# Performance work log

Hardware: AMD Instinct MI355X
Metric: run time of the kernel (lower is better)

## Reference

```python
import jax, jax.numpy as jnp
import numpy as np

# NAM: in_features independent 1->H->H->1 MLPs (FeatureNNs), batched over the
# feature dimension F instead of a Python loop of tiny kernels.
# inputs: (B, F); W1,b1: (F, H); W2: (F, H, H); b2: (F, H); W3: (F, H); b3: (F,)

def setup_inputs() -> dict:
    key = jax.random.key(0)
    ks = jax.random.split(key, 7)
    B, F, H = 8192, 128, 64
    s1 = 1.0  # fan_in = 1 for first layer
    s2 = 1.0 / np.sqrt(H)
    return {
        "inputs": jax.random.normal(ks[0], (B, F), dtype=jnp.float32),
        "W1": jax.random.normal(ks[1], (F, H), dtype=jnp.float32) * s1,
        "b1": jax.random.normal(ks[2], (F, H), dtype=jnp.float32) * 0.01,
        "W2": jax.random.normal(ks[3], (F, H, H), dtype=jnp.float32) * s2,
        "b2": jax.random.normal(ks[4], (F, H), dtype=jnp.float32) * 0.01,
        "W3": jax.random.normal(ks[5], (F, H), dtype=jnp.float32) * s2,
        "b3": jax.random.normal(ks[6], (F,), dtype=jnp.float32) * 0.01,
    }


def reference(inputs, W1, b1, W2, b2, W3, b3):
    # Layer 1: scalar input per feature -> hidden.  (B,F,1)*(F,H) -> (B,F,H)
    h1 = jax.nn.relu(inputs[:, :, None] * W1[None, :, :] + b1[None, :, :])
    # Layer 2: per-feature hidden->hidden batched matmul.
    h2 = jax.nn.relu(jnp.einsum("bfh,fhk->bfk", h1, W2) + b2[None, :, :])
    # Output layer: hidden -> scalar per feature.
    fnn = jnp.einsum("bfh,fh->bf", h2, W3) + b3[None, :]  # (B, F)
    out = fnn.sum(axis=-1)  # (B,)  additive model output
    return (out, fnn)
```

## Files before the change

### kernel.cpp

```cpp
#include <hip/hip_runtime.h>

#define B 8192
#define F 128
#define H 64

typedef __attribute__((ext_vector_type(8))) short bf16x8;
typedef __attribute__((ext_vector_type(4))) float f32x4;

static __device__ __forceinline__ unsigned short f32_to_bf16_rne(float v) {
    unsigned int u = __float_as_uint(v);
    unsigned int r = (u + 0x7FFFu + ((u >> 16) & 1u)) >> 16;
    return (unsigned short)r;
}
static __device__ __forceinline__ float bf16_to_f32(unsigned short h) {
    return __uint_as_float(((unsigned int)h) << 16);
}

#define GLOAD_LDS16(gp, lp)                                                  \
    __builtin_amdgcn_global_load_lds(                                        \
        (const __attribute__((address_space(1))) unsigned int*)(gp),         \
        (__attribute__((address_space(3))) unsigned int*)(lp), 16, 0, 0)


__global__ __launch_bounds__(256) void nam_prep(
    const float* __restrict__ inputs, const float* __restrict__ W2,
    short* __restrict__ bhi_g, short* __restrict__ blo_g,
    float* __restrict__ xT)
{
    const int tid = threadIdx.x;
    const int blk = blockIdx.x;
    __shared__ float tile[32][65];
    if (blk < 512) {
        const int r0 = (blk & 127) * 64;
        const int f0 = (blk >> 7) * 32;
#pragma unroll
        for (int j = 0; j < 8; ++j) {
            const int rl = j * 8 + (tid >> 5);
            const int fl = tid & 31;
            tile[fl][rl] = inputs[(size_t)(r0 + rl) * F + f0 + fl];
        }
        __syncthreads();
#pragma unroll
        for (int j = 0; j < 8; ++j) {
            const int fl = j * 4 + (tid >> 6);
            const int rl = tid & 63;
            xT[(size_t)(f0 + fl) * B + r0 + rl] = tile[fl][rl];
        }
    } else {
        const int f = blk - 512;
        const float* W2f = W2 + (size_t)f * H * H;
        short* bhi = bhi_g + (size_t)f * 4096;
        short* blo = blo_g + (size_t)f * 4096;
#pragma unroll
        for (int t = tid; t < 512; t += 256) {
            const int n = t & 63;
            const int g = t >> 6;
            const int nt = n >> 4, c = n & 15;
            const int ks = g >> 2, q = g & 3;
            const int slot = (nt * 2 + ks) * 64 + c + 16 * q;
            bf16x8 hv, lv;
#pragma unroll
            for (int jj = 0; jj < 8; ++jj) {
                const float wv = W2f[(g * 8 + jj) * H + n];
                const unsigned short hi = f32_to_bf16_rne(wv);
                const unsigned short lo = f32_to_bf16_rne(wv - bf16_to_f32(hi));
                hv[jj] = (short)hi;
                lv[jj] = (short)lo;
            }
            *(bf16x8*)&bhi[slot * 8] = hv;
            *(bf16x8*)&blo[slot * 8] = lv;
        }
    }
}

__global__ __launch_bounds__(256, 3) void nam_main(
    const float* __restrict__ xT, const float* __restrict__ W1,
    const float* __restrict__ b1, const short* __restrict__ bhi_g,
    const short* __restrict__ blo_g, const float* __restrict__ b2,
    const float* __restrict__ W3, const float* __restrict__ b3,
    float* __restrict__ fnn_ws)
{
    const int tid = threadIdx.x;
    const int f = blockIdx.y;
    const int b0 = blockIdx.x * 256;

    const int lane = tid & 63;
    const int w    = tid >> 6;
    const int q    = lane >> 4;
    const int col  = lane & 15;

    __shared__ __align__(16) short bhs[4096];
    __shared__ __align__(16) short bls[4096];
    {
        const short* bhi_f = bhi_g + (size_t)f * 4096;
        const short* blo_f = blo_g + (size_t)f * 4096;
#pragma unroll
        for (int c = w; c < 8; c += 4) {
            GLOAD_LDS16(bhi_f + c * 512 + lane * 8, &bhs[c * 512]);
            GLOAD_LDS16(blo_f + c * 512 + lane * 8, &bls[c * 512]);
        }
    }

    float x4[4];
#pragma unroll
    for (int mt = 0; mt < 4; ++mt)
        x4[mt] = xT[(size_t)f * B + b0 + w * 64 + mt * 16 + col];

    const float* W1f = W1 + f * H;
    const float* b1f = b1 + f * H;
    float w1v[16], b1v[16];
#pragma unroll
    for (int ks = 0; ks < 2; ++ks)
#pragma unroll
        for (int j = 0; j < 8; ++j) {
            w1v[ks * 8 + j] = W1f[ks * 32 + q * 8 + j];
            b1v[ks * 8 + j] = b1f[ks * 32 + q * 8 + j];
        }
    const float* b2f = b2 + f * H;
    const float* W3f = W3 + f * H;
    float b2v[4], w3v[4];
#pragma unroll
    for (int nt = 0; nt < 4; ++nt) {
        b2v[nt] = b2f[nt * 16 + col];
        w3v[nt] = W3f[nt * 16 + col];
    }
    const float b3f = b3[f];

    __syncthreads();

    bf16x8 bhi[4][2], blo[4][2];
#pragma unroll
    for (int nt = 0; nt < 4; ++nt)
#pragma unroll
        for (int ks = 0; ks < 2; ++ks) {
            const int slot = (nt * 2 + ks) * 64 + lane;
            bhi[nt][ks] = *(bf16x8*)&bhs[slot * 8];
            blo[nt][ks] = *(bf16x8*)&bls[slot * 8];
        }

#pragma unroll 1
    for (int mt = 0; mt < 4; ++mt) {
        const int rbase = b0 + w * 64 + mt * 16;
        const float x = x4[mt];

        f32x4 acc[4];
#pragma unroll
        for (int nt = 0; nt < 4; ++nt) {
            acc[nt][0] = b2v[nt]; acc[nt][1] = b2v[nt];
            acc[nt][2] = b2v[nt]; acc[nt][3] = b2v[nt];
        }

#pragma unroll
        for (int ks = 0; ks < 2; ++ks) {
            union { unsigned int u[4]; bf16x8 v; } Ah, Al;
#pragma unroll
            for (int t = 0; t < 4; ++t) {
                const float r0 = fmaxf(fmaf(x, w1v[ks * 8 + 2 * t],     b1v[ks * 8 + 2 * t]),     0.0f);
                const float r1 = fmaxf(fmaf(x, w1v[ks * 8 + 2 * t + 1], b1v[ks * 8 + 2 * t + 1]), 0.0f);
                const unsigned int u0 = __float_as_uint(r0);
                const unsigned int u1 = __float_as_uint(r1);
                const float l0 = r0 - __uint_as_float(u0 & 0xFFFF0000u);
                const float l1 = r1 - __uint_as_float(u1 & 0xFFFF0000u);
                Ah.u[t] = __builtin_amdgcn_perm(u1, u0, 0x07060302);
                Al.u[t] = __builtin_amdgcn_perm(__float_as_uint(l1),
                                                __float_as_uint(l0), 0x07060302);
            }
#pragma unroll
            for (int nt = 0; nt < 4; ++nt) {
                acc[nt] = __builtin_amdgcn_mfma_f32_16x16x32_bf16(Ah.v, bhi[nt][ks], acc[nt], 0, 0, 0);
                acc[nt] = __builtin_amdgcn_mfma_f32_16x16x32_bf16(Ah.v, blo[nt][ks], acc[nt], 0, 0, 0);
                acc[nt] = __builtin_amdgcn_mfma_f32_16x16x32_bf16(Al.v, bhi[nt][ks], acc[nt], 0, 0, 0);
            }
        }

        float s[4];
#pragma unroll
        for (int reg = 0; reg < 4; ++reg) {
            float t = 0.0f;
#pragma unroll
            for (int nt = 0; nt < 4; ++nt)
                t = fmaf(fmaxf(acc[nt][reg], 0.0f), w3v[nt], t);
            s[reg] = t;
        }
#pragma unroll
        for (int m_ = 1; m_ <= 8; m_ <<= 1)
#pragma unroll
            for (int reg = 0; reg < 4; ++reg)
                s[reg] += __shfl_xor(s[reg], m_, 64);
        if (col == 0) {
            f32x4 o;
            o[0] = s[0] + b3f; o[1] = s[1] + b3f;
            o[2] = s[2] + b3f; o[3] = s[3] + b3f;
            *(f32x4*)&fnn_ws[(size_t)f * B + rbase + 4 * q] = o;
        }
    }
}

__global__ __launch_bounds__(256) void nam_finish(
    const float* __restrict__ fnn_ws, float* __restrict__ fnn,
    float* __restrict__ out)
{
    const int tid = threadIdx.x;
    const int blk = blockIdx.x;
    const int r0 = (blk & 127) * 64;
    const int f0 = (blk >> 7) * 32;
    __shared__ float tile[32][65];
    __shared__ float psum[4][64];

    float rsum = 0.0f;
#pragma unroll
    for (int j = 0; j < 8; ++j) {
        const int fl = j * 4 + (tid >> 6);
        const int rl = tid & 63;
        const float v = fnn_ws[(size_t)(f0 + fl) * B + r0 + rl];
        tile[fl][rl] = v;
        rsum += v;
    }
    psum[tid >> 6][tid & 63] = rsum;
    __syncthreads();
    if (tid < 64) {
        const float s = psum[0][tid] + psum[1][tid] + psum[2][tid] + psum[3][tid];
        atomicAdd(&out[r0 + tid], s);
    }
#pragma unroll
    for (int j = 0; j < 8; ++j) {
        const int rl = j * 8 + (tid >> 5);
        const int fl = tid & 31;
        fnn[(size_t)(r0 + rl) * F + f0 + fl] = tile[fl][rl];
    }
}

__global__ __launch_bounds__(256, 3) void nam_mono(
    const float* __restrict__ inputs, const float* __restrict__ W1,
    const float* __restrict__ b1, const float* __restrict__ W2,
    const float* __restrict__ b2, const float* __restrict__ W3,
    const float* __restrict__ b3, float* __restrict__ out,
    float* __restrict__ fnn_out)
{
    const int tid = threadIdx.x;
    const int f = blockIdx.y;
    const int b0 = blockIdx.x * 256;

    const float* W1f = W1 + f * H;
    const float* b1f = b1 + f * H;
    const float* W2f = W2 + (size_t)f * H * H;
    const float* b2f = b2 + f * H;
    const float* W3f = W3 + f * H;

    __shared__ __align__(16) short bhi_s[512 * 8];
    __shared__ __align__(16) short blo_s[512 * 8];

#pragma unroll
    for (int t = tid; t < 512; t += 256) {
        const int n = t & 63;
        const int g = t >> 6;
        const int nt = n >> 4, c = n & 15;
        const int ks = g >> 2, q = g & 3;
        const int slot = (nt * 2 + ks) * 64 + c + 16 * q;
        bf16x8 hv, lv;
#pragma unroll
        for (int jj = 0; jj < 8; ++jj) {
            const float wv = W2f[(g * 8 + jj) * H + n];
            const unsigned short hi = f32_to_bf16_rne(wv);
            const unsigned short lo = f32_to_bf16_rne(wv - bf16_to_f32(hi));
            hv[jj] = (short)hi;
            lv[jj] = (short)lo;
        }
        *(bf16x8*)&bhi_s[slot * 8] = hv;
        *(bf16x8*)&blo_s[slot * 8] = lv;
    }

    const int lane = tid & 63;
    const int w    = tid >> 6;
    const int q    = lane >> 4;
    const int col  = lane & 15;

    float w1v[16], b1v[16];
#pragma unroll
    for (int ks = 0; ks < 2; ++ks)
#pragma unroll
        for (int j = 0; j < 8; ++j) {
            w1v[ks * 8 + j] = W1f[ks * 32 + q * 8 + j];
            b1v[ks * 8 + j] = b1f[ks * 32 + q * 8 + j];
        }
    float b2v[4], w3v[4];
#pragma unroll
    for (int nt = 0; nt < 4; ++nt) {
        b2v[nt] = b2f[nt * 16 + col];
        w3v[nt] = W3f[nt * 16 + col];
    }
    const float b3f = b3[f];

    float x4[4];
#pragma unroll
    for (int mt = 0; mt < 4; ++mt)
        x4[mt] = inputs[(size_t)(b0 + w * 64 + mt * 16 + col) * F + f];

    __syncthreads();

    bf16x8 bhi[4][2], blo[4][2];
#pragma unroll
    for (int nt = 0; nt < 4; ++nt)
#pragma unroll
        for (int ks = 0; ks < 2; ++ks) {
            const int slot = (nt * 2 + ks) * 64 + lane;
            bhi[nt][ks] = *(bf16x8*)&bhi_s[slot * 8];
            blo[nt][ks] = *(bf16x8*)&blo_s[slot * 8];
        }

#pragma unroll 1
    for (int mt = 0; mt < 4; ++mt) {
        const int rbase = b0 + w * 64 + mt * 16;
        const float x = x4[mt];

        f32x4 acc[4];
#pragma unroll
        for (int nt = 0; nt < 4; ++nt) {
            acc[nt][0] = b2v[nt]; acc[nt][1] = b2v[nt];
            acc[nt][2] = b2v[nt]; acc[nt][3] = b2v[nt];
        }

#pragma unroll
        for (int ks = 0; ks < 2; ++ks) {
            union { unsigned int u[4]; bf16x8 v; } Ah, Al;
#pragma unroll
            for (int t = 0; t < 4; ++t) {
                const float r0 = fmaxf(fmaf(x, w1v[ks * 8 + 2 * t],     b1v[ks * 8 + 2 * t]),     0.0f);
                const float r1 = fmaxf(fmaf(x, w1v[ks * 8 + 2 * t + 1], b1v[ks * 8 + 2 * t + 1]), 0.0f);
                const unsigned int u0 = __float_as_uint(r0);
                const unsigned int u1 = __float_as_uint(r1);
                const float l0 = r0 - __uint_as_float(u0 & 0xFFFF0000u);
                const float l1 = r1 - __uint_as_float(u1 & 0xFFFF0000u);
                Ah.u[t] = __builtin_amdgcn_perm(u1, u0, 0x07060302);
                Al.u[t] = __builtin_amdgcn_perm(__float_as_uint(l1),
                                                __float_as_uint(l0), 0x07060302);
            }
#pragma unroll
            for (int nt = 0; nt < 4; ++nt) {
                acc[nt] = __builtin_amdgcn_mfma_f32_16x16x32_bf16(Ah.v, bhi[nt][ks], acc[nt], 0, 0, 0);
                acc[nt] = __builtin_amdgcn_mfma_f32_16x16x32_bf16(Ah.v, blo[nt][ks], acc[nt], 0, 0, 0);
                acc[nt] = __builtin_amdgcn_mfma_f32_16x16x32_bf16(Al.v, bhi[nt][ks], acc[nt], 0, 0, 0);
            }
        }

        float s[4];
#pragma unroll
        for (int reg = 0; reg < 4; ++reg) {
            float t = 0.0f;
#pragma unroll
            for (int nt = 0; nt < 4; ++nt)
                t = fmaf(fmaxf(acc[nt][reg], 0.0f), w3v[nt], t);
            s[reg] = t;
        }
#pragma unroll
        for (int m_ = 1; m_ <= 8; m_ <<= 1)
#pragma unroll
            for (int reg = 0; reg < 4; ++reg)
                s[reg] += __shfl_xor(s[reg], m_, 64);
        if (col == 0) {
#pragma unroll
            for (int reg = 0; reg < 4; ++reg) {
                const int row = rbase + 4 * q + reg;
                const float val = s[reg] + b3f;
                fnn_out[(size_t)row * F + f] = val;
                atomicAdd(&out[row], val);
            }
        }
    }
}

extern "C" void kernel_launch(void* const* d_in, const int* in_sizes, int n_in,
                              void* d_out, int out_size, void* d_ws, size_t ws_size,
                              hipStream_t stream) {
    const float* inputs = (const float*)d_in[0];
    const float* W1     = (const float*)d_in[1];
    const float* b1     = (const float*)d_in[2];
    const float* W2     = (const float*)d_in[3];
    const float* b2     = (const float*)d_in[4];
    const float* W3     = (const float*)d_in[5];
    const float* b3     = (const float*)d_in[6];

    float* out = (float*)d_out;
    float* fnn = out + B;

    const size_t WS_NEEDED = (size_t)F * 4096 * 2 * sizeof(short)
                           + (size_t)F * B * 2 * sizeof(float);

    hipMemsetAsync(out, 0, B * sizeof(float), stream);

    if (ws_size >= WS_NEEDED) {
        short* bhi_g = (short*)d_ws;
        short* blo_g = bhi_g + (size_t)F * 4096;
        float* xT    = (float*)(blo_g + (size_t)F * 4096);
        float* fnw   = xT + (size_t)F * B;

        nam_prep<<<dim3(512 + F), 256, 0, stream>>>(inputs, W2, bhi_g, blo_g, xT);
        nam_main<<<dim3(B / 256, F), 256, 0, stream>>>(xT, W1, b1, bhi_g, blo_g,
                                                       b2, W3, b3, fnw);
        nam_finish<<<dim3(512), 256, 0, stream>>>(fnw, fnn, out);
    } else {
        nam_mono<<<dim3(B / 256, F), 256, 0, stream>>>(inputs, W1, b1, W2, b2,
                                                       W3, b3, out, fnn);
    }
}
```

Measured before the change: 107.5 us.

## Drop input transpose pass, read inputs strided in main kernel, raise occupancy

Removes the transpose of inputs into a feature-major workspace buffer from the prep kernel, so prep now only converts W2 into hi/lo bf16 fragments. The main kernel reads each x value straight from the row-major inputs with stride F, which saves a full read and write of the 4 MB input array but makes those loads uncoalesced. It also raises the launch-bounds occupancy hint from 3 to 4 blocks and unrolls the row-tile loop by 2, which adds register pressure. There is a harmless redundant self-assignment line in the lo conversion.

```diff
diff --git a/kernel.cpp b/kernel.cpp
--- a/kernel.cpp
+++ b/kernel.cpp
@@ -23,58 +23,38 @@
 
 
 __global__ __launch_bounds__(256) void nam_prep(
-    const float* __restrict__ inputs, const float* __restrict__ W2,
-    short* __restrict__ bhi_g, short* __restrict__ blo_g,
-    float* __restrict__ xT)
+    const float* __restrict__ W2, short* __restrict__ bhi_g,
+    short* __restrict__ blo_g)
 {
     const int tid = threadIdx.x;
-    const int blk = blockIdx.x;
-    __shared__ float tile[32][65];
-    if (blk < 512) {
-        const int r0 = (blk & 127) * 64;
-        const int f0 = (blk >> 7) * 32;
-#pragma unroll
-        for (int j = 0; j < 8; ++j) {
-            const int rl = j * 8 + (tid >> 5);
-            const int fl = tid & 31;
-            tile[fl][rl] = inputs[(size_t)(r0 + rl) * F + f0 + fl];
-        }
-        __syncthreads();
-#pragma unroll
-        for (int j = 0; j < 8; ++j) {
-            const int fl = j * 4 + (tid >> 6);
-            const int rl = tid & 63;
-            xT[(size_t)(f0 + fl) * B + r0 + rl] = tile[fl][rl];
-        }
-    } else {
-        const int f = blk - 512;
-        const float* W2f = W2 + (size_t)f * H * H;
-        short* bhi = bhi_g + (size_t)f * 4096;
-        short* blo = blo_g + (size_t)f * 4096;
-#pragma unroll
-        for (int t = tid; t < 512; t += 256) {
-            const int n = t & 63;
-            const int g = t >> 6;
-            const int nt = n >> 4, c = n & 15;
-            const int ks = g >> 2, q = g & 3;
-            const int slot = (nt * 2 + ks) * 64 + c + 16 * q;
-            bf16x8 hv, lv;
-#pragma unroll
-            for (int jj = 0; jj < 8; ++jj) {
-                const float wv = W2f[(g * 8 + jj) * H + n];
-                const unsigned short hi = f32_to_bf16_rne(wv);
-                const unsigned short lo = f32_to_bf16_rne(wv - bf16_to_f32(hi));
-                hv[jj] = (short)hi;
-                lv[jj] = (short)lo;
-            }
-            *(bf16x8*)&bhi[slot * 8] = hv;
-            *(bf16x8*)&blo[slot * 8] = lv;
-        }
-    }
-}
-
-__global__ __launch_bounds__(256, 3) void nam_main(
-    const float* __restrict__ xT, const float* __restrict__ W1,
+    const int f = blockIdx.x;
+    const float* W2f = W2 + (size_t)f * H * H;
+    short* bhi = bhi_g + (size_t)f * 4096;
+    short* blo = blo_g + (size_t)f * 4096;
+#pragma unroll
+    for (int t = tid; t < 512; t += 256) {
+        const int n = t & 63;
+        const int g = t >> 6;
+        const int nt = n >> 4, c = n & 15;
+        const int ks = g >> 2, q = g & 3;
+        const int slot = (nt * 2 + ks) * 64 + c + 16 * q;
+        bf16x8 hv, lv;
+#pragma unroll
+        for (int jj = 0; jj < 8; ++jj) {
+            const float wv = W2f[(g * 8 + jj) * H + n];
+            const unsigned short hi = f32_to_bf16_rne(wv);
+            const unsigned short lo = f32_to_bf16_rne(wv - bf16_to_f32(hi));
+            hv[jj] = (short)hi;
+            lv[jj] = (short)lv[jj];
+            lv[jj] = (short)lo;
+        }
+        *(bf16x8*)&bhi[slot * 8] = hv;
+        *(bf16x8*)&blo[slot * 8] = lv;
+    }
+}
+
+__global__ __launch_bounds__(256, 4) void nam_main(
+    const float* __restrict__ inputs, const float* __restrict__ W1,
     const float* __restrict__ b1, const short* __restrict__ bhi_g,
     const short* __restrict__ blo_g, const float* __restrict__ b2,
     const float* __restrict__ W3, const float* __restrict__ b3,
@@ -104,7 +84,7 @@
     float x4[4];
 #pragma unroll
     for (int mt = 0; mt < 4; ++mt)
-        x4[mt] = xT[(size_t)f * B + b0 + w * 64 + mt * 16 + col];
+        x4[mt] = inputs[(size_t)(b0 + w * 64 + mt * 16 + col) * F + f];
 
     const float* W1f = W1 + f * H;
     const float* b1f = b1 + f * H;
@@ -138,7 +118,7 @@
             blo[nt][ks] = *(bf16x8*)&bls[slot * 8];
         }
 
-#pragma unroll 1
+#pragma unroll 2
     for (int mt = 0; mt < 4; ++mt) {
         const int rbase = b0 + w * 64 + mt * 16;
         const float x = x4[mt];
@@ -384,19 +364,18 @@
     float* fnn = out + B;
 
     const size_t WS_NEEDED = (size_t)F * 4096 * 2 * sizeof(short)
-                           + (size_t)F * B * 2 * sizeof(float);
+                           + (size_t)F * B * sizeof(float);
 
     hipMemsetAsync(out, 0, B * sizeof(float), stream);
 
     if (ws_size >= WS_NEEDED) {
         short* bhi_g = (short*)d_ws;
         short* blo_g = bhi_g + (size_t)F * 4096;
-        float* xT    = (float*)(blo_g + (size_t)F * 4096);
-        float* fnw   = xT + (size_t)F * B;
-
-        nam_prep<<<dim3(512 + F), 256, 0, stream>>>(inputs, W2, bhi_g, blo_g, xT);
-        nam_main<<<dim3(B / 256, F), 256, 0, stream>>>(xT, W1, b1, bhi_g, blo_g,
-                                                       b2, W3, b3, fnw);
+        float* fnw   = (float*)(blo_g + (size_t)F * 4096);
+
+        nam_prep<<<dim3(F), 256, 0, stream>>>(W2, bhi_g, blo_g);
+        nam_main<<<dim3(B / 256, F), 256, 0, stream>>>(inputs, W1, b1, bhi_g,
+                                                       blo_g, b2, W3, b3, fnw);
         nam_finish<<<dim3(512), 256, 0, stream>>>(fnw, fnn, out);
     } else {
         nam_mono<<<dim3(B / 256, F), 256, 0, stream>>>(inputs, W1, b1, W2, b2,
```

After: 203.4 us. 89.3% more time.
